# Optimization experiments

Measured on AMD Instinct MI355X. Metric: run time of the kernel, lower is better.

## Reference

```python
import jax, jax.numpy as jnp
import numpy as np

B, N, IN_F, OUT_F, H = 4, 2048, 128, 128, 4
D = OUT_F // H  # head_dim = 32
NEG_SLOPE = 0.2


def setup_inputs() -> dict:
    key = jax.random.key(0)
    k1, k2, k3, k4, k5 = jax.random.split(key, 5)
    x = jax.random.normal(k1, (B, N, IN_F), dtype=jnp.float32)
    adj = jax.random.randint(k2, (N, N), 0, 2, dtype=jnp.int32)
    adj = adj.at[jnp.arange(N), jnp.arange(N)].set(1)  # self-loops
    # xavier-uniform-like init
    lim_w = float(np.sqrt(6.0 / (IN_F + OUT_F)))
    W = jax.random.uniform(k3, (OUT_F, IN_F), minval=-lim_w, maxval=lim_w, dtype=jnp.float32)
    lim_a = float(np.sqrt(6.0 / (H + D)))
    a_src = jax.random.uniform(k4, (H, D), minval=-lim_a, maxval=lim_a, dtype=jnp.float32)
    a_dst = jax.random.uniform(k5, (H, D), minval=-lim_a, maxval=lim_a, dtype=jnp.float32)
    return {"x": x, "adj": adj, "W": W, "a_src": a_src, "a_dst": a_dst}


def reference(x, adj, W, a_src, a_dst):
    Bx, Nx, _ = x.shape
    # linear projection: (B,N,out) -> (B,N,H,D)
    h = jnp.einsum('bni,oi->bno', x, W).reshape(Bx, Nx, H, D)
    e_src = jnp.einsum('bnhd,hd->bnh', h, a_src)  # (B,N,H)
    e_dst = jnp.einsum('bnhd,hd->bnh', h, a_dst)  # (B,N,H)
    # scores: (B,N_src,H,N_dst)
    scores = jax.nn.leaky_relu(
        e_src[:, :, :, None] + e_dst.transpose(0, 2, 1)[:, None, :, :],
        negative_slope=NEG_SLOPE,
    )
    mask = adj[None, :, None, :]  # (1,N,1,N)
    scores = jnp.where(mask == 0, -jnp.inf, scores)
    attn = jax.nn.softmax(scores, axis=-1)  # (B,N,H,N); dropout is identity at eval
    out = jnp.einsum('bnhm,bmhd->bnhd', attn, h)  # (B,N,H,D)
    return out.reshape(Bx, Nx, H * D)
```

## Files before the change

### kernel.cpp

```cpp
#include <hip/hip_runtime.h>
#include <math.h>

#define BB 4
#define NN 2048
#define FF 128
#define HH 4
#define DD 32
#define NEG_SLOPE 0.2f
#define LOG2E 1.4426950408889634f

typedef __attribute__((ext_vector_type(8))) short short8;
typedef __attribute__((ext_vector_type(4))) float floatx4;

__device__ __forceinline__ float exp2_fast(float x) {
#if __has_builtin(__builtin_amdgcn_exp2f)
    return __builtin_amdgcn_exp2f(x);
#else
    return exp2f(x);
#endif
}

__global__ __launch_bounds__(256) void k_gemm_h(const float* __restrict__ x,
                                                const float* __restrict__ W,
                                                float* __restrict__ h) {
    __shared__ float xs[16][FF];
    __shared__ float wt[32][132];
    int t = threadIdx.x;
    long rows0 = (long)blockIdx.x * 16;
#pragma unroll
    for (int k = 0; k < 2; ++k) {
        int q = t + k * 256;
        int r = q >> 5, c4 = q & 31;
        float4 v = ((const float4*)(x + (rows0 + r) * FF))[c4];
        *(float4*)&xs[r][c4 * 4] = v;
    }
    int og = t & 31, rg = t >> 5;
    float acc[2][4];
#pragma unroll
    for (int a = 0; a < 2; ++a)
#pragma unroll
        for (int c = 0; c < 4; ++c) acc[a][c] = 0.f;

    int wo = t & 127, wg = t >> 7;
    for (int i0 = 0; i0 < FF; i0 += 32) {
        __syncthreads();
#pragma unroll
        for (int u = 0; u < 4; ++u) {
            float4 v = *(const float4*)(W + (long)wo * FF + i0 + wg * 16 + u * 4);
            wt[wg * 16 + u * 4 + 0][wo] = v.x;
            wt[wg * 16 + u * 4 + 1][wo] = v.y;
            wt[wg * 16 + u * 4 + 2][wo] = v.z;
            wt[wg * 16 + u * 4 + 3][wo] = v.w;
        }
        __syncthreads();
#pragma unroll
        for (int i = 0; i < 32; ++i) {
            float4 w4 = *(const float4*)&wt[i][og * 4];
            float x0 = xs[rg * 2 + 0][i0 + i];
            float x1 = xs[rg * 2 + 1][i0 + i];
            acc[0][0] += x0 * w4.x; acc[0][1] += x0 * w4.y;
            acc[0][2] += x0 * w4.z; acc[0][3] += x0 * w4.w;
            acc[1][0] += x1 * w4.x; acc[1][1] += x1 * w4.y;
            acc[1][2] += x1 * w4.z; acc[1][3] += x1 * w4.w;
        }
    }
#pragma unroll
    for (int a = 0; a < 2; ++a) {
        float4 o4 = {acc[a][0], acc[a][1], acc[a][2], acc[a][3]};
        *(float4*)(h + (rows0 + rg * 2 + a) * FF + og * 4) = o4;
    }
}

__global__ __launch_bounds__(256) void k_edges(const float* __restrict__ h,
                                               const float* __restrict__ a_src,
                                               const float* __restrict__ a_dst,
                                               float* __restrict__ es_t,
                                               float* __restrict__ ed_t) {
    __shared__ float as_[HH * DD], ad_[HH * DD];
    int t = threadIdx.x;
    if (t < HH * DD) { as_[t] = a_src[t]; ad_[t] = a_dst[t]; }
    __syncthreads();
    int g = blockIdx.x * 256 + t;
    int hh = g & (HH - 1);
    int n  = (g >> 2) & (NN - 1);
    int b  = g >> 13;
    const float* hp = h + ((long)(b * NN + n)) * FF + hh * DD;
    float es = 0.f, ed = 0.f;
#pragma unroll
    for (int d4 = 0; d4 < DD / 4; ++d4) {
        float4 v = ((const float4*)hp)[d4];
        float4 s = *(const float4*)&as_[hh * DD + d4 * 4];
        float4 d = *(const float4*)&ad_[hh * DD + d4 * 4];
        es += v.x * s.x + v.y * s.y + v.z * s.z + v.w * s.w;
        ed += v.x * d.x + v.y * d.y + v.z * d.z + v.w * d.w;
    }
    es_t[(b * HH + hh) * NN + n] = es * LOG2E;
    ed_t[(b * HH + hh) * NN + n] = ed * LOG2E;
}

__global__ __launch_bounds__(256) void k_pack_adj(const int* __restrict__ adj,
                                                  unsigned int* __restrict__ bits) {
    int idx = blockIdx.x * 256 + threadIdx.x;
    int n = idx >> 6, w = idx & 63;
    const int4* base = (const int4*)(adj + (size_t)n * NN + w * 32);
    unsigned int word = 0;
#pragma unroll
    for (int q = 0; q < 8; ++q) {
        int4 a = base[q];
        word |= ((unsigned int)(a.x & 1)) << (q * 4 + 0);
        word |= ((unsigned int)(a.y & 1)) << (q * 4 + 1);
        word |= ((unsigned int)(a.z & 1)) << (q * 4 + 2);
        word |= ((unsigned int)(a.w & 1)) << (q * 4 + 3);
    }
    bits[idx] = word;
}


__global__ __launch_bounds__(256) void k_ht(const float* __restrict__ h,
                                            unsigned short* __restrict__ ht) {
    __shared__ unsigned short tile[DD][136];
    int t = threadIdx.x;
    int m0 = blockIdx.x * 128;
    int bh = blockIdx.y;
    int b = bh >> 2, head = bh & 3;
    int m_l = t >> 1, g = (t & 1) * 16;
    const float* hp = h + ((long)(b * NN + m0 + m_l)) * FF + head * DD + g;
#pragma unroll
    for (int u = 0; u < 4; ++u) {
        float4 v = *(const float4*)(hp + u * 4);
#pragma unroll
        for (int e = 0; e < 4; ++e) {
            float f = (&v.x)[e];
            unsigned int ui = __float_as_uint(f);
            ui += 0x7FFFu + ((ui >> 16) & 1u);
            tile[g + u * 4 + e][m_l] = (unsigned short)(ui >> 16);
        }
    }
    __syncthreads();
    int d = t >> 3, c = t & 7;
    unsigned short* op = ht + ((size_t)bh * DD + d) * NN + m0;
#pragma unroll
    for (int k = 0; k < 2; ++k) {
        int4 v = *(const int4*)&tile[d][(c + k * 8) * 8];
        *(int4*)(op + (c + k * 8) * 8) = v;
    }
}

#define HSTRIDE 2056
__global__ __launch_bounds__(512, 2) void k_attn(
        const unsigned short* __restrict__ ht,
        const unsigned int* __restrict__ bits,
        const float* __restrict__ es_t,
        const float* __restrict__ ed_t,
        float* __restrict__ out) {
    __shared__ unsigned short hb[DD * HSTRIDE];
    __shared__ float eds[NN];
    int t = threadIdx.x;
    int n0 = blockIdx.x * 128;
    int bh = blockIdx.y;
    int b = bh >> 2, head = bh & 3;

    {
        float4 v = ((const float4*)(ed_t + (size_t)bh * NN))[t];
        *(float4*)&eds[t * 4] = v;
    }
    {
        const unsigned short* htp = ht + (size_t)bh * DD * NN;
        int d = t >> 4, c = t & 15;
#pragma unroll
        for (int k = 0; k < 16; ++k) {
            int ch = c + k * 16;
            int4 v = *(const int4*)(htp + (size_t)d * NN + ch * 8);
            *(int4*)&hb[d * HSTRIDE + ch * 8] = v;
        }
    }
    __syncthreads();

    int wid = t >> 6, lane = t & 63;
    int q = lane >> 4, r = lane & 15;
    int n = n0 + wid * 16 + r;
    float es = es_t[(size_t)bh * NN + n];
    const unsigned int* brow = bits + (size_t)n * (NN / 32);

    floatx4 acc0 = {0.f, 0.f, 0.f, 0.f};
    floatx4 acc1 = {0.f, 0.f, 0.f, 0.f};
    floatx4 accd = {0.f, 0.f, 0.f, 0.f};
    union { short8 s8; int i[4]; } ones;
    ones.i[0] = 0x3F803F80; ones.i[1] = 0x3F803F80;
    ones.i[2] = 0x3F803F80; ones.i[3] = 0x3F803F80;

    int qo = q * 8;
#pragma unroll 2
    for (int m0 = 0; m0 < NN; m0 += 32) {
        unsigned int word = brow[m0 >> 5];
        float4 e0 = *(const float4*)&eds[m0 + qo];
        float4 e1 = *(const float4*)&eds[m0 + qo + 4];
        float w[8];
#pragma unroll
        for (int j = 0; j < 8; ++j) {
            float ev = j < 4 ? (&e0.x)[j] : (&e1.x)[j - 4];
            float s = es + ev;
            float l = fmaxf(s, NEG_SLOPE * s);
            float v = exp2_fast(l);
            unsigned int bit = (word >> (qo + j)) & 1u;
            unsigned int msk = 0u - bit;
            w[j] = __uint_as_float(__float_as_uint(v) & msk);
        }
        union { short8 s8; int i[4]; } af;
#pragma unroll
        for (int p = 0; p < 4; ++p)
            af.i[p] = __builtin_amdgcn_perm(__float_as_uint(w[2 * p + 1]),
                                            __float_as_uint(w[2 * p]),
                                            0x07060302u);
        short8 b0 = *(const short8*)&hb[r * HSTRIDE + m0 + qo];
        short8 b1 = *(const short8*)&hb[(16 + r) * HSTRIDE + m0 + qo];
        acc0 = __builtin_amdgcn_mfma_f32_16x16x32_bf16(af.s8, b0, acc0, 0, 0, 0);
        acc1 = __builtin_amdgcn_mfma_f32_16x16x32_bf16(af.s8, b1, acc1, 0, 0, 0);
        accd = __builtin_amdgcn_mfma_f32_16x16x32_bf16(af.s8, ones.s8, accd, 0, 0, 0);
    }

#pragma unroll
    for (int reg = 0; reg < 4; ++reg) {
        int nrow = n0 + wid * 16 + q * 4 + reg;
        float inv = 1.0f / accd[reg];
        float* op = out + ((size_t)(b * NN + nrow)) * FF + head * DD;
        op[r]      = acc0[reg] * inv;
        op[16 + r] = acc1[reg] * inv;
    }
}

extern "C" void kernel_launch(void* const* d_in, const int* in_sizes, int n_in,
                              void* d_out, int out_size, void* d_ws, size_t ws_size,
                              hipStream_t stream) {
    const float* x     = (const float*)d_in[0];
    const int*   adj   = (const int*)d_in[1];
    const float* W     = (const float*)d_in[2];
    const float* a_src = (const float*)d_in[3];
    const float* a_dst = (const float*)d_in[4];
    float* out = (float*)d_out;

    float* h    = (float*)d_ws;
    float* es_t = h + (size_t)BB * NN * FF;
    float* ed_t = es_t + (size_t)BB * HH * NN;
    unsigned int* bits = (unsigned int*)(ed_t + (size_t)BB * HH * NN);
    unsigned short* ht = (unsigned short*)(bits + (size_t)NN * (NN / 32));

    hipLaunchKernelGGL(k_pack_adj, dim3(NN * (NN / 32) / 256), dim3(256), 0, stream,
                       adj, bits);
    hipLaunchKernelGGL(k_gemm_h, dim3(BB * NN / 16), dim3(256), 0, stream, x, W, h);
    hipLaunchKernelGGL(k_edges, dim3(BB * NN * HH / 256), dim3(256), 0, stream,
                       h, a_src, a_dst, es_t, ed_t);
    hipLaunchKernelGGL(k_ht, dim3(NN / 128, BB * HH), dim3(256), 0, stream, h, ht);
    hipLaunchKernelGGL(k_attn, dim3(NN / 128, BB * HH), dim3(512), 0, stream,
                       ht, bits, es_t, ed_t, out);
}
```

Measured before the change: 111.6 us.

## Fuse projection, edge scores and bf16 transpose; stage attention tiles in halves

Merges the GEMM, edge-score and bf16 transpose kernels into one kernel, so the fp32 h buffer is never written to or read back from global memory. Edge scores are reduced with warp shuffles, and the bf16 transposed h is written straight out from a small shared tile. The attention kernel now stages h in two swizzled halves to cut LDS size and bank conflicts, caches adjacency bit words in shared memory, and drops the min-2-blocks launch bound. The extra sync and reload between halves may add stalls, and the fused GEMM epilogue does more work per block.

```diff
diff --git a/kernel.cpp b/kernel.cpp
--- a/kernel.cpp
+++ b/kernel.cpp
@@ -20,13 +20,43 @@
 #endif
 }
 
-__global__ __launch_bounds__(256) void k_gemm_h(const float* __restrict__ x,
-                                                const float* __restrict__ W,
-                                                float* __restrict__ h) {
+__device__ __forceinline__ unsigned short to_bf16(float f) {
+    unsigned int ui = __float_as_uint(f);
+    ui += 0x7FFFu + ((ui >> 16) & 1u);
+    return (unsigned short)(ui >> 16);
+}
+
+__global__ __launch_bounds__(256) void k_pack_adj(const int* __restrict__ adj,
+                                                  unsigned int* __restrict__ bits) {
+    int idx = blockIdx.x * 256 + threadIdx.x;
+    int n = idx >> 6, w = idx & 63;
+    const int4* base = (const int4*)(adj + (size_t)n * NN + w * 32);
+    unsigned int word = 0;
+#pragma unroll
+    for (int q = 0; q < 8; ++q) {
+        int4 a = base[q];
+        word |= ((unsigned int)(a.x & 1)) << (q * 4 + 0);
+        word |= ((unsigned int)(a.y & 1)) << (q * 4 + 1);
+        word |= ((unsigned int)(a.z & 1)) << (q * 4 + 2);
+        word |= ((unsigned int)(a.w & 1)) << (q * 4 + 3);
+    }
+    bits[idx] = word;
+}
+
+__global__ __launch_bounds__(256) void k_gemm_fused(const float* __restrict__ x,
+                                                    const float* __restrict__ W,
+                                                    const float* __restrict__ a_src,
+                                                    const float* __restrict__ a_dst,
+                                                    unsigned short* __restrict__ ht,
+                                                    float* __restrict__ es_t,
+                                                    float* __restrict__ ed_t) {
     __shared__ float xs[16][FF];
     __shared__ float wt[32][132];
+    __shared__ float as_s[FF], ad_s[FF];
+    __shared__ unsigned short tile2[16][136];
     int t = threadIdx.x;
     long rows0 = (long)blockIdx.x * 16;
+    if (t < FF) { as_s[t] = a_src[t]; ad_s[t] = a_dst[t]; }
 #pragma unroll
     for (int k = 0; k < 2; ++k) {
         int q = t + k * 256;
@@ -64,123 +94,75 @@
             acc[1][2] += x1 * w4.z; acc[1][3] += x1 * w4.w;
         }
     }
-#pragma unroll
-    for (int a = 0; a < 2; ++a) {
-        float4 o4 = {acc[a][0], acc[a][1], acc[a][2], acc[a][3]};
-        *(float4*)(h + (rows0 + rg * 2 + a) * FF + og * 4) = o4;
-    }
-}
-
-__global__ __launch_bounds__(256) void k_edges(const float* __restrict__ h,
-                                               const float* __restrict__ a_src,
-                                               const float* __restrict__ a_dst,
-                                               float* __restrict__ es_t,
-                                               float* __restrict__ ed_t) {
-    __shared__ float as_[HH * DD], ad_[HH * DD];
-    int t = threadIdx.x;
-    if (t < HH * DD) { as_[t] = a_src[t]; ad_[t] = a_dst[t]; }
+
+    int head = og >> 3;
+    int b = (int)(rows0 >> 11);
+    int m_block = (int)(rows0 & 2047);
+    float es0 = 0.f, ed0 = 0.f, es1 = 0.f, ed1 = 0.f;
+#pragma unroll
+    for (int c = 0; c < 4; ++c) {
+        int col = og * 4 + c;
+        es0 += acc[0][c] * as_s[col]; ed0 += acc[0][c] * ad_s[col];
+        es1 += acc[1][c] * as_s[col]; ed1 += acc[1][c] * ad_s[col];
+    }
+#pragma unroll
+    for (int k = 1; k < 8; k <<= 1) {
+        es0 += __shfl_xor(es0, k); ed0 += __shfl_xor(ed0, k);
+        es1 += __shfl_xor(es1, k); ed1 += __shfl_xor(ed1, k);
+    }
+    if ((og & 7) == 0) {
+        size_t eb = (size_t)(b * HH + head) * NN + m_block + rg * 2;
+        es_t[eb]     = es0 * LOG2E; ed_t[eb]     = ed0 * LOG2E;
+        es_t[eb + 1] = es1 * LOG2E; ed_t[eb + 1] = ed1 * LOG2E;
+    }
+
+#pragma unroll
+    for (int a = 0; a < 2; ++a)
+#pragma unroll
+        for (int c = 0; c < 4; ++c)
+            tile2[rg * 2 + a][og * 4 + c] = to_bf16(acc[a][c]);
     __syncthreads();
-    int g = blockIdx.x * 256 + t;
-    int hh = g & (HH - 1);
-    int n  = (g >> 2) & (NN - 1);
-    int b  = g >> 13;
-    const float* hp = h + ((long)(b * NN + n)) * FF + hh * DD;
-    float es = 0.f, ed = 0.f;
-#pragma unroll
-    for (int d4 = 0; d4 < DD / 4; ++d4) {
-        float4 v = ((const float4*)hp)[d4];
-        float4 s = *(const float4*)&as_[hh * DD + d4 * 4];
-        float4 d = *(const float4*)&ad_[hh * DD + d4 * 4];
-        es += v.x * s.x + v.y * s.y + v.z * s.z + v.w * s.w;
-        ed += v.x * d.x + v.y * d.y + v.z * d.z + v.w * d.w;
-    }
-    es_t[(b * HH + hh) * NN + n] = es * LOG2E;
-    ed_t[(b * HH + hh) * NN + n] = ed * LOG2E;
-}
-
-__global__ __launch_bounds__(256) void k_pack_adj(const int* __restrict__ adj,
-                                                  unsigned int* __restrict__ bits) {
-    int idx = blockIdx.x * 256 + threadIdx.x;
-    int n = idx >> 6, w = idx & 63;
-    const int4* base = (const int4*)(adj + (size_t)n * NN + w * 32);
-    unsigned int word = 0;
-#pragma unroll
-    for (int q = 0; q < 8; ++q) {
-        int4 a = base[q];
-        word |= ((unsigned int)(a.x & 1)) << (q * 4 + 0);
-        word |= ((unsigned int)(a.y & 1)) << (q * 4 + 1);
-        word |= ((unsigned int)(a.z & 1)) << (q * 4 + 2);
-        word |= ((unsigned int)(a.w & 1)) << (q * 4 + 3);
-    }
-    bits[idx] = word;
-}
-
-
-__global__ __launch_bounds__(256) void k_ht(const float* __restrict__ h,
-                                            unsigned short* __restrict__ ht) {
-    __shared__ unsigned short tile[DD][136];
-    int t = threadIdx.x;
-    int m0 = blockIdx.x * 128;
-    int bh = blockIdx.y;
-    int b = bh >> 2, head = bh & 3;
-    int m_l = t >> 1, g = (t & 1) * 16;
-    const float* hp = h + ((long)(b * NN + m0 + m_l)) * FF + head * DD + g;
-#pragma unroll
-    for (int u = 0; u < 4; ++u) {
-        float4 v = *(const float4*)(hp + u * 4);
-#pragma unroll
-        for (int e = 0; e < 4; ++e) {
-            float f = (&v.x)[e];
-            unsigned int ui = __float_as_uint(f);
-            ui += 0x7FFFu + ((ui >> 16) & 1u);
-            tile[g + u * 4 + e][m_l] = (unsigned short)(ui >> 16);
-        }
-    }
-    __syncthreads();
-    int d = t >> 3, c = t & 7;
-    unsigned short* op = ht + ((size_t)bh * DD + d) * NN + m0;
-#pragma unroll
-    for (int k = 0; k < 2; ++k) {
-        int4 v = *(const int4*)&tile[d][(c + k * 8) * 8];
-        *(int4*)(op + (c + k * 8) * 8) = v;
-    }
-}
-
-#define HSTRIDE 2056
-__global__ __launch_bounds__(512, 2) void k_attn(
+    {
+        int cg = t >> 1, half = t & 1;
+        int d = cg & 31, hd = cg >> 5;
+        unsigned short tmp[8];
+#pragma unroll
+        for (int j = 0; j < 8; ++j) tmp[j] = tile2[half * 8 + j][cg];
+        unsigned short* op = ht + ((size_t)(b * HH + hd) * DD + d) * NN + m_block + half * 8;
+        *(int4*)op = *(const int4*)tmp;
+    }
+}
+
+#define HB_HALF 1024
+__global__ __launch_bounds__(512) void k_attn(
         const unsigned short* __restrict__ ht,
         const unsigned int* __restrict__ bits,
         const float* __restrict__ es_t,
         const float* __restrict__ ed_t,
         float* __restrict__ out) {
-    __shared__ unsigned short hb[DD * HSTRIDE];
+    __shared__ unsigned short hb[DD * HB_HALF];
     __shared__ float eds[NN];
+    __shared__ unsigned int bitw[128][68];
     int t = threadIdx.x;
     int n0 = blockIdx.x * 128;
     int bh = blockIdx.y;
     int b = bh >> 2, head = bh & 3;
 
-    {
-        float4 v = ((const float4*)(ed_t + (size_t)bh * NN))[t];
-        *(float4*)&eds[t * 4] = v;
-    }
-    {
-        const unsigned short* htp = ht + (size_t)bh * DD * NN;
-        int d = t >> 4, c = t & 15;
-#pragma unroll
-        for (int k = 0; k < 16; ++k) {
-            int ch = c + k * 16;
-            int4 v = *(const int4*)(htp + (size_t)d * NN + ch * 8);
-            *(int4*)&hb[d * HSTRIDE + ch * 8] = v;
-        }
-    }
-    __syncthreads();
+    ((float4*)eds)[t] = ((const float4*)(ed_t + (size_t)bh * NN))[t];
+#pragma unroll
+    for (int k = 0; k < 4; ++k) {
+        int q = t + k * 512;
+        int nl = q >> 4, wq = q & 15;
+        int4 v = ((const int4*)(bits + (size_t)(n0 + nl) * 64))[wq];
+        *(int4*)&bitw[nl][wq * 4] = v;
+    }
 
     int wid = t >> 6, lane = t & 63;
     int q = lane >> 4, r = lane & 15;
-    int n = n0 + wid * 16 + r;
-    float es = es_t[(size_t)bh * NN + n];
-    const unsigned int* brow = bits + (size_t)n * (NN / 32);
+    int qo = q * 8, sw = r & 7;
+    int n_l = wid * 16 + r;
+    float es = es_t[(size_t)bh * NN + n0 + n_l];
+    const unsigned short* htp = ht + (size_t)bh * DD * NN;
 
     floatx4 acc0 = {0.f, 0.f, 0.f, 0.f};
     floatx4 acc1 = {0.f, 0.f, 0.f, 0.f};
@@ -189,34 +171,45 @@
     ones.i[0] = 0x3F803F80; ones.i[1] = 0x3F803F80;
     ones.i[2] = 0x3F803F80; ones.i[3] = 0x3F803F80;
 
-    int qo = q * 8;
+    for (int half = 0; half < 2; ++half) {
+        __syncthreads();
+#pragma unroll
+        for (int k = 0; k < 8; ++k) {
+            int qq = t + k * 512;
+            int d = qq >> 7, cm = qq & 127;
+            int4 v = *(const int4*)(htp + (size_t)d * NN + half * HB_HALF + cm * 8);
+            *(int4*)&hb[d * HB_HALF + ((cm ^ (d & 7)) * 8)] = v;
+        }
+        __syncthreads();
+        const unsigned int* brow = bitw[n_l];
 #pragma unroll 2
-    for (int m0 = 0; m0 < NN; m0 += 32) {
-        unsigned int word = brow[m0 >> 5];
-        float4 e0 = *(const float4*)&eds[m0 + qo];
-        float4 e1 = *(const float4*)&eds[m0 + qo + 4];
-        float w[8];
-#pragma unroll
-        for (int j = 0; j < 8; ++j) {
-            float ev = j < 4 ? (&e0.x)[j] : (&e1.x)[j - 4];
-            float s = es + ev;
-            float l = fmaxf(s, NEG_SLOPE * s);
-            float v = exp2_fast(l);
-            unsigned int bit = (word >> (qo + j)) & 1u;
-            unsigned int msk = 0u - bit;
-            w[j] = __uint_as_float(__float_as_uint(v) & msk);
-        }
-        union { short8 s8; int i[4]; } af;
-#pragma unroll
-        for (int p = 0; p < 4; ++p)
-            af.i[p] = __builtin_amdgcn_perm(__float_as_uint(w[2 * p + 1]),
-                                            __float_as_uint(w[2 * p]),
-                                            0x07060302u);
-        short8 b0 = *(const short8*)&hb[r * HSTRIDE + m0 + qo];
-        short8 b1 = *(const short8*)&hb[(16 + r) * HSTRIDE + m0 + qo];
-        acc0 = __builtin_amdgcn_mfma_f32_16x16x32_bf16(af.s8, b0, acc0, 0, 0, 0);
-        acc1 = __builtin_amdgcn_mfma_f32_16x16x32_bf16(af.s8, b1, acc1, 0, 0, 0);
-        accd = __builtin_amdgcn_mfma_f32_16x16x32_bf16(af.s8, ones.s8, accd, 0, 0, 0);
+        for (int m0 = 0; m0 < HB_HALF; m0 += 32) {
+            int mg = half * HB_HALF + m0;
+            unsigned int word = brow[mg >> 5];
+            float4 e0 = *(const float4*)&eds[mg + qo];
+            float4 e1 = *(const float4*)&eds[mg + qo + 4];
+            float w[8];
+#pragma unroll
+            for (int j = 0; j < 8; ++j) {
+                float ev = j < 4 ? (&e0.x)[j] : (&e1.x)[j - 4];
+                float s = es + ev;
+                float l = fmaxf(s, NEG_SLOPE * s);
+                float v = exp2_fast(l);
+                w[j] = (word & (1u << (qo + j))) ? v : 0.f;
+            }
+            union { short8 s8; int i[4]; } af;
+#pragma unroll
+            for (int p = 0; p < 4; ++p)
+                af.i[p] = __builtin_amdgcn_perm(__float_as_uint(w[2 * p + 1]),
+                                                __float_as_uint(w[2 * p]),
+                                                0x07060302u);
+            int cs = ((m0 + qo) >> 3) ^ sw;
+            short8 b0 = *(const short8*)&hb[r * HB_HALF + cs * 8];
+            short8 b1 = *(const short8*)&hb[(16 + r) * HB_HALF + cs * 8];
+            acc0 = __builtin_amdgcn_mfma_f32_16x16x32_bf16(af.s8, b0, acc0, 0, 0, 0);
+            acc1 = __builtin_amdgcn_mfma_f32_16x16x32_bf16(af.s8, b1, acc1, 0, 0, 0);
+            accd = __builtin_amdgcn_mfma_f32_16x16x32_bf16(af.s8, ones.s8, accd, 0, 0, 0);
+        }
     }
 
 #pragma unroll
@@ -239,18 +232,15 @@
     const float* a_dst = (const float*)d_in[4];
     float* out = (float*)d_out;
 
-    float* h    = (float*)d_ws;
-    float* es_t = h + (size_t)BB * NN * FF;
+    float* es_t = (float*)d_ws;
     float* ed_t = es_t + (size_t)BB * HH * NN;
     unsigned int* bits = (unsigned int*)(ed_t + (size_t)BB * HH * NN);
     unsigned short* ht = (unsigned short*)(bits + (size_t)NN * (NN / 32));
 
     hipLaunchKernelGGL(k_pack_adj, dim3(NN * (NN / 32) / 256), dim3(256), 0, stream,
                        adj, bits);
-    hipLaunchKernelGGL(k_gemm_h, dim3(BB * NN / 16), dim3(256), 0, stream, x, W, h);
-    hipLaunchKernelGGL(k_edges, dim3(BB * NN * HH / 256), dim3(256), 0, stream,
-                       h, a_src, a_dst, es_t, ed_t);
-    hipLaunchKernelGGL(k_ht, dim3(NN / 128, BB * HH), dim3(256), 0, stream, h, ht);
+    hipLaunchKernelGGL(k_gemm_fused, dim3(BB * NN / 16), dim3(256), 0, stream,
+                       x, W, a_src, a_dst, ht, es_t, ed_t);
     hipLaunchKernelGGL(k_attn, dim3(NN / 128, BB * HH), dim3(512), 0, stream,
                        ht, bits, es_t, ed_t, out);
 }
```

Result: faster. 106.3 us (-4.8%).
